# Performance work log

Hardware: AMD Instinct MI355X
Metric: run time of the kernel (lower is better)

Reference implementation:

```python
import jax, jax.numpy as jnp
import numpy as np

NUM_ITERATIONS = 3
LN_EPS = 1e-5


def setup_inputs() -> dict:
    key = jax.random.key(0)
    ks = jax.random.split(key, 10)
    B, L, Lv, H = 8, 2048, 256, 1024
    s = 1.0 / np.sqrt(H)
    s2 = 1.0 / np.sqrt(2 * H)
    return {
        "text_feat": jax.random.normal(ks[0], (B, L, H), dtype=jnp.float32),
        "vision_feat": jax.random.normal(ks[1], (B, Lv, H), dtype=jnp.float32),
        "Wt": jax.random.uniform(ks[2], (H, H), jnp.float32, -s, s),
        "bt": jax.random.uniform(ks[3], (H,), jnp.float32, -s, s),
        "Wv": jax.random.uniform(ks[4], (H, H), jnp.float32, -s, s),
        "bv": jax.random.uniform(ks[5], (H,), jnp.float32, -s, s),
        "Wg": jax.random.uniform(ks[6], (H, 2 * H), jnp.float32, -s2, s2),
        "bg": jax.random.uniform(ks[7], (H,), jnp.float32, -s2, s2),
        "gamma": jnp.ones((H,), jnp.float32),
        "beta": jnp.zeros((H,), jnp.float32),
    }


def reference(text_feat, vision_feat, Wt, bt, Wv, bv, Wg, bg, gamma, beta):
    B, L, H = text_feat.shape
    # mean-pool vision over its sequence, broadcast over L
    vision_pooled = jnp.mean(vision_feat, axis=1, keepdims=True)          # [B,1,H]
    text_proj = jnp.einsum('blh,oh->blo', text_feat, Wt) + bt             # [B,L,H]
    vision_proj = jnp.einsum('bkh,oh->bko', vision_pooled, Wv) + bv       # [B,1,H]
    vision_proj = jnp.broadcast_to(vision_proj, (B, L, H))                # expand to [B,L,H]

    # agreement is loop-invariant in the original code; compute once
    agreement = jnp.sum(text_proj * vision_proj, axis=-1, keepdims=True)  # [B,L,1]

    coupling = jnp.zeros((B, L, 1), dtype=text_feat.dtype)
    fused = text_feat
    for _ in range(NUM_ITERATIONS):
        routing_weights = jax.nn.softmax(coupling, axis=1)                # softmax over L
        weighted_vision = routing_weights * vision_proj                   # [B,L,H]
        # gate = sigmoid(Linear(concat(text_proj, weighted_vision)))
        Wg_t, Wg_v = Wg[:, :H], Wg[:, H:]
        gate_pre = (jnp.einsum('blh,oh->blo', text_proj, Wg_t)
                    + jnp.einsum('blh,oh->blo', weighted_vision, Wg_v) + bg)
        gate = jax.nn.sigmoid(gate_pre)
        fused = text_feat + gate * weighted_vision
        coupling = coupling + agreement

    # LayerNorm over last dim (dropout is identity in eval)
    mu = jnp.mean(fused, axis=-1, keepdims=True)
    var = jnp.mean(jnp.square(fused - mu), axis=-1, keepdims=True)
    out = (fused - mu) / jnp.sqrt(var + LN_EPS) * gamma + beta
    return out
```

## Files before the change

kernel.cpp:

```cpp
#include <hip/hip_runtime.h>
#include <hip/hip_bf16.h>
#include <hip/hip_fp8.h>

typedef __bf16 bf16_t;
typedef bf16_t bf16x4 __attribute__((ext_vector_type(4)));
typedef bf16_t bf16x8 __attribute__((ext_vector_type(8)));
typedef float  f32x4  __attribute__((ext_vector_type(4)));

#define B_  8
#define L_  2048
#define H_  1024
#define LV_ 256

typedef const __attribute__((address_space(1))) void* gptr_as1;
typedef __attribute__((address_space(3))) void* lptr_as3;

__device__ __forceinline__ void gload_lds16(void* lds_base, const void* gsrc) {
  __builtin_amdgcn_global_load_lds((gptr_as1)gsrc, (lptr_as3)lds_base, 16, 0, 0);
}
__device__ __forceinline__ void gload_lds4(void* lds_base, const void* gsrc) {
  __builtin_amdgcn_global_load_lds((gptr_as1)gsrc, (lptr_as3)lds_base, 4, 0, 0);
}

__device__ __forceinline__ unsigned char to_fp8(float x) {
  return __hip_fp8_e4m3(x).__x;
}

__global__ __launch_bounds__(256) void vpool64(const float* __restrict__ vf,
                                               float* __restrict__ pooled) {
  __shared__ float part[256];
  int bid = blockIdx.x;
  int b = bid >> 3, hc = bid & 7;
  int t = threadIdx.x;
  int h = hc * 128 + (t & 127);
  int kh = t >> 7;
  const float* p = vf + (long)b * (LV_ * H_) + (long)kh * 128 * H_ + h;
  float s = 0.f;
  #pragma unroll 4
  for (int k = 0; k < 128; ++k) s += p[k * H_];
  part[t] = s;
  __syncthreads();
  if (t < 128)
    pooled[b * H_ + hc * 128 + t] = (part[t] + part[t + 128]) * (1.f / 256.f);
}

__global__ void matvec8(const float* __restrict__ W, int ldw, int woff,
                        const float* __restrict__ x,
                        const float* __restrict__ bias,
                        float* __restrict__ out) {
  int wid = threadIdx.x >> 6, lane = threadIdx.x & 63;
  int o = blockIdx.x * 4 + wid;
  const float* wr = W + (long)o * ldw + woff;
  float acc[B_];
  #pragma unroll
  for (int b = 0; b < B_; ++b) acc[b] = 0.f;
  for (int j = 0; j < 16; ++j) {
    float w = wr[lane + 64 * j];
    #pragma unroll
    for (int b = 0; b < B_; ++b) acc[b] += w * x[b * H_ + lane + 64 * j];
  }
  #pragma unroll
  for (int b = 0; b < B_; ++b)
    for (int off = 32; off; off >>= 1) acc[b] += __shfl_down(acc[b], off);
  if (lane == 0) {
    float bb = bias ? bias[o] : 0.f;
    #pragma unroll
    for (int b = 0; b < B_; ++b) out[b * H_ + o] = acc[b] + bb;
  }
}

__global__ __launch_bounds__(256) void smallops(const float* __restrict__ Wg,
                                                const float* __restrict__ Wt,
                                                const float* __restrict__ vp,
                                                const float* __restrict__ bt,
                                                const float* __restrict__ bg,
                                                float* __restrict__ gv,
                                                float* __restrict__ partU,
                                                float* __restrict__ cbb) {
  int bid = blockIdx.x;
  if (bid < 256) {
    int wid = threadIdx.x >> 6, lane = threadIdx.x & 63;
    int o = bid * 4 + wid;
    const float* wr = Wg + (long)o * 2048 + 1024;
    float acc[B_];
    #pragma unroll
    for (int b = 0; b < B_; ++b) acc[b] = 0.f;
    for (int j = 0; j < 16; ++j) {
      float w = wr[lane + 64 * j];
      #pragma unroll
      for (int b = 0; b < B_; ++b) acc[b] += w * vp[b * H_ + lane + 64 * j];
    }
    #pragma unroll
    for (int b = 0; b < B_; ++b)
      for (int off = 32; off; off >>= 1) acc[b] += __shfl_down(acc[b], off);
    if (lane == 0) {
      #pragma unroll
      for (int b = 0; b < B_; ++b) gv[b * H_ + o] = acc[b];
    }
  } else if (bid < 512) {
    int lb = bid - 256;
    int e = (lb & 3) * 256 + threadIdx.x;
    int oc = lb >> 2;
    float a[B_];
    #pragma unroll
    for (int b = 0; b < B_; ++b) a[b] = 0.f;
    #pragma unroll
    for (int i = 0; i < 16; ++i) {
      int o = oc * 16 + i;
      float w = Wt[(long)o * H_ + e];
      #pragma unroll
      for (int b = 0; b < B_; ++b) a[b] += w * vp[b * H_ + o];
    }
    #pragma unroll
    for (int b = 0; b < B_; ++b) partU[oc * 8192 + b * 1024 + e] = a[b];
  } else {
    int lb = bid - 512;
    int wid = threadIdx.x >> 6, lane = threadIdx.x & 63;
    int o = lb * 4 + wid;
    const float* wr = Wg + (long)o * 2048;
    float acc = 0.f;
    for (int j = 0; j < 16; ++j) acc += wr[lane + 64 * j] * bt[lane + 64 * j];
    for (int off = 32; off; off >>= 1) acc += __shfl_down(acc, off);
    if (lane == 0) cbb[o] = acc + bg[o];
  }
}

__global__ __launch_bounds__(256) void reduceK(const float* __restrict__ src,
                                               float* __restrict__ dst,
                                               int nc, float scale) {
  int j = blockIdx.x * 256 + threadIdx.x;
  float s = 0.f;
  for (int c = 0; c < nc; ++c) s += src[c * 8192 + j];
  dst[j] = s * scale;
}

__global__ __launch_bounds__(256) void cvt_pack(const float* __restrict__ text,
                                                const float* __restrict__ u,
                                                const float* __restrict__ Wt,
                                                unsigned char* __restrict__ t8p,
                                                float* __restrict__ agr,
                                                bf16_t* __restrict__ WtT) {
  int bid = blockIdx.x;
  int t = threadIdx.x;
  if (bid < 1024) {
    __shared__ unsigned char q8[16][1032];
    __shared__ float dred[4][16];
    int b = bid >> 7;
    int wid = t >> 6, lane = t & 63;
    const float4* trow = (const float4*)(text + (long)bid * (16 * H_));
    float4 uu = ((const float4*)(u + b * H_))[t];
    #pragma unroll 4
    for (int i = 0; i < 16; ++i) {
      float4 v = trow[i * 256 + t];
      float d = v.x * uu.x + v.y * uu.y + v.z * uu.z + v.w * uu.w;
      for (int off = 32; off; off >>= 1) d += __shfl_down(d, off);
      if (!lane) dred[wid][i] = d;
      uchar4 q = { to_fp8(v.x), to_fp8(v.y), to_fp8(v.z), to_fp8(v.w) };
      *(uchar4*)&q8[i][t * 4] = q;
    }
    __syncthreads();
    if (t < 16)
      agr[bid * 16 + t] = dred[0][t] + dred[1][t] + dred[2][t] + dred[3][t];
    unsigned char* dst = t8p + (long)bid * 16384;
    #pragma unroll
    for (int c = 0; c < 8; ++c) {
      int kb = wid * 8 + c;
      uint2 r = *(const uint2*)&q8[lane & 15][kb * 32 + (lane >> 4) * 8];
      *(uint2*)(dst + kb * 512 + lane * 8) = r;
    }
  } else {
    __shared__ float tile[64][65];
    int lb = bid - 1024;
    int hr = (lb >> 4) * 64;
    int ec = (lb & 15) * 64;
    int lr = t >> 4, lc = t & 15;
    #pragma unroll
    for (int rr = 0; rr < 4; ++rr) {
      int r = rr * 16 + lr;
      float4 v = *(const float4*)(Wt + (long)(hr + r) * H_ + ec + lc * 4);
      tile[r][lc * 4 + 0] = v.x; tile[r][lc * 4 + 1] = v.y;
      tile[r][lc * 4 + 2] = v.z; tile[r][lc * 4 + 3] = v.w;
    }
    __syncthreads();
    #pragma unroll
    for (int rr = 0; rr < 4; ++rr) {
      int er = rr * 16 + lr;
      bf16x4 o = { (bf16_t)tile[lc * 4 + 0][er], (bf16_t)tile[lc * 4 + 1][er],
                   (bf16_t)tile[lc * 4 + 2][er], (bf16_t)tile[lc * 4 + 3][er] };
      *(bf16x4*)(WtT + (long)(ec + er) * H_ + hr + lc * 4) = o;
    }
  }
}

__global__ __launch_bounds__(256) void wc_sm(const float* __restrict__ Wg,
                                             const bf16_t* __restrict__ Bt,
                                             unsigned char* __restrict__ Cw8,
                                             const float* __restrict__ ag,
                                             float* __restrict__ r) {
  __shared__ __align__(16) char lds[2][16384];
  __shared__ float red[4];
  if (blockIdx.x >= 256) {
    int b = blockIdx.x - 256, t = threadIdx.x;
    int wid = t >> 6, lane = t & 63;
    const float* a = ag + (long)b * L_;
    float v[8];
    float mx = -1e30f;
    #pragma unroll
    for (int j = 0; j < 8; ++j) { v[j] = 2.f * a[t + 256 * j]; mx = fmaxf(mx, v[j]); }
    for (int off = 32; off; off >>= 1) mx = fmaxf(mx, __shfl_down(mx, off));
    if (!lane) red[wid] = mx;
    __syncthreads();
    mx = fmaxf(fmaxf(red[0], red[1]), fmaxf(red[2], red[3]));
    __syncthreads();
    float sum = 0.f;
    #pragma unroll
    for (int j = 0; j < 8; ++j) { v[j] = __expf(v[j] - mx); sum += v[j]; }
    for (int off = 32; off; off >>= 1) sum += __shfl_down(sum, off);
    if (!lane) red[wid] = sum;
    __syncthreads();
    sum = red[0] + red[1] + red[2] + red[3];
    float inv = 1.f / sum;
    #pragma unroll
    for (int j = 0; j < 8; ++j) r[(long)b * L_ + t + 256 * j] = v[j] * inv;
    return;
  }
  const int tid = threadIdx.x;
  const int wid = tid >> 6, lane = tid & 63;
  const int fr = lane & 15, fkb = (lane >> 4) * 16, fq = (lane >> 4) * 4;
  const int wm = wid >> 1, wn = wid & 1;
  const int tm = blockIdx.x & 15, tn = blockIdx.x >> 4;
  const int m0 = tm * 64, n0 = tn * 64;

  const int d0 = tid * 16;
  const int p  = d0 ^ (((d0 >> 7) & 7) << 4);
  const int rS = p >> 7, cS = (p & 127) >> 1;

  const int swz = (fr & 7) << 4;
  const int e0 = fkb ^ swz;
  const int e1 = (64 + fkb) ^ swz;

  auto stage = [&](int t) {
    char* base = lds[t & 1];
    gload_lds16(base + 8192 + d0,        Bt + (long)(n0 + rS) * H_ + t * 64 + cS);
    gload_lds16(base + 8192 + 4096 + d0, Bt + (long)(n0 + 32 + rS) * H_ + t * 64 + cS);
    const float* a0 = Wg + (long)(m0 + rS) * 2048 + t * 64 + cS;
    const float* a1 = Wg + (long)(m0 + 32 + rS) * 2048 + t * 64 + cS;
    float4 x0 = *(const float4*)a0, x1 = *(const float4*)(a0 + 4);
    float4 y0 = *(const float4*)a1, y1 = *(const float4*)(a1 + 4);
    bf16x8 bx = { (bf16_t)x0.x, (bf16_t)x0.y, (bf16_t)x0.z, (bf16_t)x0.w,
                  (bf16_t)x1.x, (bf16_t)x1.y, (bf16_t)x1.z, (bf16_t)x1.w };
    bf16x8 by = { (bf16_t)y0.x, (bf16_t)y0.y, (bf16_t)y0.z, (bf16_t)y0.w,
                  (bf16_t)y1.x, (bf16_t)y1.y, (bf16_t)y1.z, (bf16_t)y1.w };
    *(bf16x8*)(base + d0) = bx;
    *(bf16x8*)(base + 4096 + d0) = by;
  };

  f32x4 acc[2][2];
  #pragma unroll
  for (int m = 0; m < 2; ++m)
    #pragma unroll
    for (int n = 0; n < 2; ++n) acc[m][n] = (f32x4){0.f, 0.f, 0.f, 0.f};

  stage(0);
  __syncthreads();
  for (int t = 0; t < 16; ++t) {
    if (t + 1 < 16) stage(t + 1);
    char* buf = lds[t & 1];
    char* AR = buf + (wm * 32 + fr) * 128;
    char* BR = buf + 8192 + (wn * 32 + fr) * 128;
    bf16x8 a[2][2], b[2][2];
    #pragma unroll
    for (int m = 0; m < 2; ++m) {
      a[m][0] = *(const bf16x8*)(AR + m * 2048 + e0);
      a[m][1] = *(const bf16x8*)(AR + m * 2048 + e1);
      b[m][0] = *(const bf16x8*)(BR + m * 2048 + e0);
      b[m][1] = *(const bf16x8*)(BR + m * 2048 + e1);
    }
    #pragma unroll
    for (int m = 0; m < 2; ++m)
      #pragma unroll
      for (int n = 0; n < 2; ++n) {
        acc[m][n] = __builtin_amdgcn_mfma_f32_16x16x32_bf16(a[m][0], b[n][0], acc[m][n], 0, 0, 0);
        acc[m][n] = __builtin_amdgcn_mfma_f32_16x16x32_bf16(a[m][1], b[n][1], acc[m][n], 0, 0, 0);
      }
    __syncthreads();
  }
  #pragma unroll
  for (int m = 0; m < 2; ++m)
    #pragma unroll
    for (int r_ = 0; r_ < 4; ++r_) {
      int row = m0 + wm * 32 + m * 16 + fq + r_;
      #pragma unroll
      for (int n = 0; n < 2; ++n) {
        int col = n0 + wn * 32 + n * 16 + fr;
        Cw8[((row >> 4) * 32 + (col >> 5)) * 512
            + ((row & 15) + (((col >> 3) & 3) << 4)) * 8 + (col & 7)]
          = to_fp8(acc[m][n][r_] * 16.f);
      }
    }
}

#define BOFF 16777216
__global__ __launch_bounds__(512, 2)
void gemm_ln(const unsigned char* __restrict__ AB,
             const float* __restrict__ textf,
             const float* __restrict__ cbb, const float* __restrict__ rbuf,
             const float* __restrict__ gvb, const float* __restrict__ vpb,
             const float* __restrict__ gamma, const float* __restrict__ beta,
             float* __restrict__ out) {
  extern __shared__ __align__(16) char dlds[];
  float* pS  = (float*)(dlds + 104448);
  float* pQ  = (float*)(dlds + 106496);
  float* muA = (float*)(dlds + 108544);
  float* invA= (float*)(dlds + 108800);
  const int tid  = threadIdx.x;
  const int w    = tid >> 6;
  const int lane = tid & 63;
  const int fr   = lane & 15;
  const int fq   = (lane >> 4) * 4;
  const int bid  = blockIdx.x;
  const long m0  = (long)bid * 64;

  const int o0 = tid * 4;
  const unsigned char* aSrc = AB + (long)bid * 65536 + (o0 >> 9) * 16384 + (o0 & 511);
  const unsigned char* bSrc = AB + BOFF + (long)(tid >> 5) * 16384 + (tid & 31) * 16;
  const int bD = (tid >> 5) * 512 + (tid & 31) * 16;

  f32x4 acc[4][8];
  #pragma unroll
  for (int m = 0; m < 4; ++m)
    #pragma unroll
    for (int n = 0; n < 8; ++n) acc[m][n] = (f32x4){0.f, 0.f, 0.f, 0.f};

#define STAGE(t)                                                        \
  {                                                                     \
    gload_lds4(dlds + ((t) % 3) * 2048 + o0, aSrc + (t) * 512);         \
    _Pragma("unroll")                                                   \
    for (int r_ = 0; r_ < 4; ++r_)                                      \
      gload_lds16(dlds + 6144 + ((t) % 3) * 32768 + r_ * 8192 + bD,     \
                  bSrc + (long)r_ * 262144 + (t) * 512);                \
  }
#define KITER(t, WN)                                                    \
  {                                                                     \
    __builtin_amdgcn_sched_barrier(0);                                  \
    asm volatile("s_waitcnt vmcnt(" #WN ")" ::: "memory");              \
    __builtin_amdgcn_s_barrier();                                       \
    __builtin_amdgcn_sched_barrier(0);                                  \
    if ((t) + 2 < 32) STAGE((t) + 2)                                    \
    const char* Ab_ = dlds + ((t) % 3) * 2048 + lane * 8;               \
    const char* Bb_ = dlds + 6144 + ((t) % 3) * 32768 + w * 4096        \
                           + lane * 8;                                  \
    long a_[4], b_[8];                                                  \
    _Pragma("unroll")                                                   \
    for (int m_ = 0; m_ < 4; ++m_)                                      \
      a_[m_] = *(const long*)(Ab_ + m_ * 512);                          \
    _Pragma("unroll")                                                   \
    for (int n_ = 0; n_ < 8; ++n_)                                      \
      b_[n_] = *(const long*)(Bb_ + n_ * 512);                          \
    _Pragma("unroll")                                                   \
    for (int m_ = 0; m_ < 4; ++m_)                                      \
      _Pragma("unroll")                                                 \
      for (int n_ = 0; n_ < 8; ++n_)                                    \
        acc[m_][n_] = __builtin_amdgcn_mfma_f32_16x16x32_fp8_fp8(       \
            a_[m_], b_[n_], acc[m_][n_], 0, 0, 0);                      \
  }

  STAGE(0)
  asm volatile("" ::: "memory");
  STAGE(1)

  KITER(0, 5)  KITER(1, 5)  KITER(2, 5)  KITER(3, 5)
  KITER(4, 5)  KITER(5, 5)  KITER(6, 5)  KITER(7, 5)
  KITER(8, 5)  KITER(9, 5)  KITER(10, 5) KITER(11, 5)
  KITER(12, 5) KITER(13, 5) KITER(14, 5) KITER(15, 5)
  KITER(16, 5) KITER(17, 5) KITER(18, 5) KITER(19, 5)
  KITER(20, 5) KITER(21, 5) KITER(22, 5) KITER(23, 5)
  KITER(24, 5) KITER(25, 5) KITER(26, 5) KITER(27, 5)
  KITER(28, 5) KITER(29, 5) KITER(30, 5) KITER(31, 0)
#undef KITER
#undef STAGE

  const int bat = (int)(m0 >> 11);
  const float* gvr = gvb + bat * H_;
  const float* vpr = vpb + bat * H_;
  float cb_[8], gv_[8], vp_[8];
  #pragma unroll
  for (int n = 0; n < 8; ++n) {
    int col = w * 128 + n * 16 + fr;
    cb_[n] = cbb[col]; gv_[n] = gvr[col]; vp_[n] = vpr[col];
  }
  #pragma unroll
  for (int m = 0; m < 4; ++m) {
    #pragma unroll
    for (int r = 0; r < 4; ++r) {
      int rl = m * 16 + fq + r;
      long row = m0 + rl;
      const float rv = rbuf[row];
      const float* tf = textf + row * H_;
      float s = 0.f, q = 0.f;
      #pragma unroll
      for (int n = 0; n < 8; ++n) {
        int col = w * 128 + n * 16 + fr;
        float gp = acc[m][n][r] * 0.0625f + cb_[n] + rv * gv_[n];
        float g = 1.f / (1.f + __expf(-gp));
        float f = tf[col] + g * rv * vp_[n];
        acc[m][n][r] = f;
        s += f; q += f * f;
      }
      #pragma unroll
      for (int off = 1; off < 16; off <<= 1) {
        s += __shfl_xor(s, off);
        q += __shfl_xor(q, off);
      }
      if (fr == 0) {
        pS[rl * 8 + w] = s;
        pQ[rl * 8 + w] = q;
      }
    }
  }
  __syncthreads();
  if (tid < 64) {
    float S = 0.f, Q = 0.f;
    #pragma unroll
    for (int w2 = 0; w2 < 8; ++w2) { S += pS[tid * 8 + w2]; Q += pQ[tid * 8 + w2]; }
    float mu = S * (1.f / H_);
    float var = Q * (1.f / H_) - mu * mu;
    muA[tid] = mu;
    invA[tid] = rsqrtf(var + 1e-5f);
  }
  __syncthreads();
  #pragma unroll
  for (int m = 0; m < 4; ++m) {
    #pragma unroll
    for (int r = 0; r < 4; ++r) {
      int rl = m * 16 + fq + r;
      float mu = muA[rl], inv = invA[rl];
      float* op = out + (m0 + rl) * H_;
      #pragma unroll
      for (int n = 0; n < 8; ++n) {
        int col = w * 128 + n * 16 + fr;
        op[col] = (acc[m][n][r] - mu) * inv * gamma[col] + beta[col];
      }
    }
  }
}

extern "C" void kernel_launch(void* const* d_in, const int* in_sizes, int n_in,
                              void* d_out, int out_size, void* d_ws, size_t ws_size,
                              hipStream_t stream) {
  const float* text  = (const float*)d_in[0];
  const float* vis   = (const float*)d_in[1];
  const float* Wt    = (const float*)d_in[2];
  const float* bt    = (const float*)d_in[3];
  const float* Wv    = (const float*)d_in[4];
  const float* bv    = (const float*)d_in[5];
  const float* Wg    = (const float*)d_in[6];
  const float* bg    = (const float*)d_in[7];
  const float* gamma = (const float*)d_in[8];
  const float* beta  = (const float*)d_in[9];
  float* out = (float*)d_out;

  char* ws = (char*)d_ws;
  unsigned char* t8p   = (unsigned char*)(ws);
  unsigned char* Wc8p  = (unsigned char*)(ws + (size_t)16777216);
  bf16_t* WtT_b = (bf16_t*)(ws + (size_t)17825792);
  float*  pooled = (float*)(ws + (size_t)19922944);
  float*  vp     = (float*)(ws + (size_t)19955712);
  float*  gv     = (float*)(ws + (size_t)19988480);
  float*  u      = (float*)(ws + (size_t)20021248);
  float*  cbb    = (float*)(ws + (size_t)20054016);
  float*  rbuf   = (float*)(ws + (size_t)20058112);
  float*  agr    = (float*)(ws + (size_t)20123648);
  float*  partU  = (float*)(ws + (size_t)20189184);

  static bool smem_set = false;
  if (!smem_set) {
    (void)hipFuncSetAttribute((const void*)gemm_ln,
                              hipFuncAttributeMaxDynamicSharedMemorySize, 109056);
    smem_set = true;
  }

  vpool64<<<64, 256, 0, stream>>>(vis, pooled);
  matvec8<<<256, 256, 0, stream>>>(Wv, 1024, 0, pooled, bv, vp);
  smallops<<<768, 256, 0, stream>>>(Wg, Wt, vp, bt, bg, gv, partU, cbb);
  reduceK<<<32, 256, 0, stream>>>(partU, u, 64, 1.f);

  cvt_pack<<<1280, 256, 0, stream>>>(text, u, Wt, t8p, agr, WtT_b);
  wc_sm<<<264, 256, 0, stream>>>(Wg, WtT_b, Wc8p, agr, rbuf);

  gemm_ln<<<256, 512, 109056, stream>>>(t8p, text, cbb, rbuf, gv, vp,
                                        gamma, beta, out);
}
```

Measured before the change: 121.0 us.

## Transpose GEMM accumulators through LDS for row-contiguous vectorized epilogue

The epilogue now stages each 16-row slice of the accumulator tile into LDS with an XOR swizzle. Each half-wavefront then owns a full row and reads text, bias, gate and vision vectors as float4 with coalesced access. LayerNorm statistics come from a single 32-lane shuffle reduction instead of cross-wave LDS partial sums, and the output is written as float4. This replaces strided scalar global loads and stores with vector accesses, at the cost of extra barriers and LDS round trips per slice.

```diff
diff --git a/kernel.cpp b/kernel.cpp
--- a/kernel.cpp
+++ b/kernel.cpp
@@ -309,10 +309,6 @@
              const float* __restrict__ gamma, const float* __restrict__ beta,
              float* __restrict__ out) {
   extern __shared__ __align__(16) char dlds[];
-  float* pS  = (float*)(dlds + 104448);
-  float* pQ  = (float*)(dlds + 106496);
-  float* muA = (float*)(dlds + 108544);
-  float* invA= (float*)(dlds + 108800);
   const int tid  = threadIdx.x;
   const int w    = tid >> 6;
   const int lane = tid & 63;
@@ -383,64 +379,70 @@
   const int bat = (int)(m0 >> 11);
   const float* gvr = gvb + bat * H_;
   const float* vpr = vpb + bat * H_;
-  float cb_[8], gv_[8], vp_[8];
-  #pragma unroll
-  for (int n = 0; n < 8; ++n) {
-    int col = w * 128 + n * 16 + fr;
-    cb_[n] = cbb[col]; gv_[n] = gvr[col]; vp_[n] = vpr[col];
-  }
+  const int lr = tid >> 5;
+  const int jj = tid & 31;
+
   #pragma unroll
   for (int m = 0; m < 4; ++m) {
-    #pragma unroll
-    for (int r = 0; r < 4; ++r) {
-      int rl = m * 16 + fq + r;
-      long row = m0 + rl;
-      const float rv = rbuf[row];
-      const float* tf = textf + row * H_;
-      float s = 0.f, q = 0.f;
-      #pragma unroll
-      for (int n = 0; n < 8; ++n) {
-        int col = w * 128 + n * 16 + fr;
-        float gp = acc[m][n][r] * 0.0625f + cb_[n] + rv * gv_[n];
-        float g = 1.f / (1.f + __expf(-gp));
-        float f = tf[col] + g * rv * vp_[n];
-        acc[m][n][r] = f;
-        s += f; q += f * f;
+    __syncthreads();
+    #pragma unroll
+    for (int n = 0; n < 8; ++n) {
+      #pragma unroll
+      for (int r = 0; r < 4; ++r) {
+        int rl = fq + r;
+        int c  = (w * 128 + n * 16 + fr) ^ (((rl >> 2) & 3) << 4);
+        *(float*)(dlds + rl * 4096 + c * 4) = acc[m][n][r];
       }
-      #pragma unroll
-      for (int off = 1; off < 16; off <<= 1) {
-        s += __shfl_xor(s, off);
-        q += __shfl_xor(q, off);
-      }
-      if (fr == 0) {
-        pS[rl * 8 + w] = s;
-        pQ[rl * 8 + w] = q;
-      }
-    }
-  }
-  __syncthreads();
-  if (tid < 64) {
-    float S = 0.f, Q = 0.f;
-    #pragma unroll
-    for (int w2 = 0; w2 < 8; ++w2) { S += pS[tid * 8 + w2]; Q += pQ[tid * 8 + w2]; }
-    float mu = S * (1.f / H_);
-    float var = Q * (1.f / H_) - mu * mu;
-    muA[tid] = mu;
-    invA[tid] = rsqrtf(var + 1e-5f);
-  }
-  __syncthreads();
-  #pragma unroll
-  for (int m = 0; m < 4; ++m) {
-    #pragma unroll
-    for (int r = 0; r < 4; ++r) {
-      int rl = m * 16 + fq + r;
-      float mu = muA[rl], inv = invA[rl];
-      float* op = out + (m0 + rl) * H_;
-      #pragma unroll
-      for (int n = 0; n < 8; ++n) {
-        int col = w * 128 + n * 16 + fr;
-        op[col] = (acc[m][n][r] - mu) * inv * gamma[col] + beta[col];
-      }
+    }
+    __syncthreads();
+    long row = m0 + m * 16 + lr;
+    float rv = rbuf[row];
+    const float* tf = textf + row * H_;
+    const int rot = ((lr >> 2) & 3) << 4;
+    float fv[32];
+    float s = 0.f, q = 0.f;
+    #pragma unroll
+    for (int k = 0; k < 8; ++k) {
+      int c0 = k * 128 + jj * 4;
+      f32x4 a4 = *(const f32x4*)(dlds + lr * 4096 + (c0 ^ rot) * 4);
+      float4 t4  = *(const float4*)(tf + c0);
+      float4 cb4 = *(const float4*)(cbb + c0);
+      float4 gv4 = *(const float4*)(gvr + c0);
+      float4 vp4 = *(const float4*)(vpr + c0);
+      float gp, g, f;
+      gp = a4[0] * 0.0625f + cb4.x + rv * gv4.x;
+      g = 1.f / (1.f + __expf(-gp));
+      f = t4.x + g * rv * vp4.x; fv[k * 4 + 0] = f; s += f; q += f * f;
+      gp = a4[1] * 0.0625f + cb4.y + rv * gv4.y;
+      g = 1.f / (1.f + __expf(-gp));
+      f = t4.y + g * rv * vp4.y; fv[k * 4 + 1] = f; s += f; q += f * f;
+      gp = a4[2] * 0.0625f + cb4.z + rv * gv4.z;
+      g = 1.f / (1.f + __expf(-gp));
+      f = t4.z + g * rv * vp4.z; fv[k * 4 + 2] = f; s += f; q += f * f;
+      gp = a4[3] * 0.0625f + cb4.w + rv * gv4.w;
+      g = 1.f / (1.f + __expf(-gp));
+      f = t4.w + g * rv * vp4.w; fv[k * 4 + 3] = f; s += f; q += f * f;
+    }
+    #pragma unroll
+    for (int off = 1; off < 32; off <<= 1) {
+      s += __shfl_xor(s, off);
+      q += __shfl_xor(q, off);
+    }
+    float mu  = s * (1.f / H_);
+    float var = q * (1.f / H_) - mu * mu;
+    float inv = rsqrtf(var + 1e-5f);
+    float* op = out + row * H_;
+    #pragma unroll
+    for (int k = 0; k < 8; ++k) {
+      int c0 = k * 128 + jj * 4;
+      float4 gg = *(const float4*)(gamma + c0);
+      float4 bb = *(const float4*)(beta + c0);
+      float4 o4;
+      o4.x = (fv[k * 4 + 0] - mu) * inv * gg.x + bb.x;
+      o4.y = (fv[k * 4 + 1] - mu) * inv * gg.y + bb.y;
+      o4.z = (fv[k * 4 + 2] - mu) * inv * gg.z + bb.z;
+      o4.w = (fv[k * 4 + 3] - mu) * inv * gg.w + bb.w;
+      *(float4*)(op + c0) = o4;
     }
   }
 }
```

New measurement: 161.6 us. 33.6% more time.
